# Kernel optimization log

Hardware: AMD Instinct MI355X
Metric: run time of the kernel (lower is better)

Reference implementation:

```python
import jax, jax.numpy as jnp
import numpy as np

N = 50000   # nodes
E = 800000  # edges
D = 256     # input feature dim
H = 128     # hidden size
OUT = 40    # output classes


def setup_inputs() -> dict:
    key = jax.random.key(0)
    ks = jax.random.split(key, 10)
    s = 0.05
    return {
        "x": jax.random.normal(ks[0], (N, D), jnp.float32),
        "edge_index": jax.random.randint(ks[1], (2, E), 0, N, dtype=jnp.int64),
        "W0": jax.random.normal(ks[2], (D, H), jnp.float32) * s,
        "b0": jnp.zeros((H,), jnp.float32),
        "W1": jax.random.normal(ks[3], (H, H), jnp.float32) * s,
        "b1": jnp.zeros((H,), jnp.float32),
        "W2": jax.random.normal(ks[4], (H, H), jnp.float32) * s,
        "b2": jnp.zeros((H,), jnp.float32),
        "Wout": jax.random.normal(ks[5], (H * 3, OUT), jnp.float32) * s,
        "bout": jnp.zeros((OUT,), jnp.float32),
    }


def _gcn_norm(edge_index, n):
    # PyG gcn_norm: add self-loops, symmetric D^-1/2 (A+I) D^-1/2 weights
    row, col = edge_index[0], edge_index[1]
    loop = jnp.arange(n, dtype=edge_index.dtype)
    row = jnp.concatenate([row, loop])
    col = jnp.concatenate([col, loop])
    deg = jax.ops.segment_sum(jnp.ones_like(col, jnp.float32), col, num_segments=n)
    dinv = jnp.where(deg > 0, jax.lax.rsqrt(jnp.maximum(deg, 1.0)), 0.0)
    norm = dinv[row] * dinv[col]  # [E+N]
    return row, col, norm


def _gcn_conv(x, W, b, row, col, norm, n):
    h = x @ W                                   # dense transform first (PyG order)
    msg = h[row] * norm[:, None]                # gather source feats, scale
    out = jax.ops.segment_sum(msg, col, num_segments=n)  # scatter-aggregate
    return out + b


def reference(x, edge_index, W0, b0, W1, b1, W2, b2, Wout, bout):
    n = x.shape[0]
    row, col, norm = _gcn_norm(edge_index, n)
    x1 = jax.nn.relu(_gcn_conv(x, W0, b0, row, col, norm, n))
    x2 = jax.nn.relu(_gcn_conv(x1, W1, b1, row, col, norm, n))
    x3 = jax.nn.relu(_gcn_conv(x2, W2, b2, row, col, norm, n))
    xs = jnp.concatenate([x1, x2, x3], axis=-1)  # JumpingKnowledge 'cat'
    return xs @ Wout + bout
```

## Files before the change

### kernel.cpp

```cpp
#include <hip/hip_runtime.h>

#define HID 128
#define NOUT 40
#define SCAN_B 256
#define NWIN 8

typedef __attribute__((ext_vector_type(8))) short bf16x8;
typedef __attribute__((ext_vector_type(4))) float f32x4;

__device__ inline float bf2f(unsigned int u) {
    unsigned int t = u << 16;
    float f;
    __builtin_memcpy(&f, &t, 4);
    return f;
}
__device__ inline unsigned short f2bf(float f) {
    unsigned int x;
    __builtin_memcpy(&x, &f, 4);
    unsigned int r = (x + 0x7fffu + ((x >> 16) & 1u)) >> 16;
    return (unsigned short)r;
}
__device__ inline bf16x8 pack_bf8(float4 u, float4 v) {
    bf16x8 r;
    r[0] = (short)f2bf(u.x); r[1] = (short)f2bf(u.y);
    r[2] = (short)f2bf(u.z); r[3] = (short)f2bf(u.w);
    r[4] = (short)f2bf(v.x); r[5] = (short)f2bf(v.y);
    r[6] = (short)f2bf(v.z); r[7] = (short)f2bf(v.w);
    return r;
}

__global__ void detect_fmt_kernel(const unsigned int* __restrict__ e, int* __restrict__ flag) {
    int t = threadIdx.x;
    unsigned int v = e[2 * t + 1];
    unsigned long long ball = __ballot(v == 0u);
    if (t == 0) *flag = (ball == ~0ull) ? 1 : 0;
}

__global__ void degree_kernel(const void* __restrict__ eix, const int* __restrict__ flag,
                              int* __restrict__ deg, int E) {
    int i = blockIdx.x * blockDim.x + threadIdx.x;
    if (i >= E) return;
    int f = *flag;
    int c = f ? (int)(((const long long*)eix)[(size_t)E + i]) : ((const int*)eix)[(size_t)E + i];
    atomicAdd(&deg[c], 1);
}

__global__ void scan1_kernel(const int* __restrict__ deg, int* __restrict__ offs,
                             int* __restrict__ bsum, float* __restrict__ dinv, int N) {
    __shared__ int s[SCAN_B];
    int i = blockIdx.x * SCAN_B + threadIdx.x;
    int v = (i < N) ? deg[i] : 0;
    if (i < N) dinv[i] = rsqrtf((float)v + 1.0f);
    s[threadIdx.x] = v;
    __syncthreads();
    for (int d = 1; d < SCAN_B; d <<= 1) {
        int t = (threadIdx.x >= d) ? s[threadIdx.x - d] : 0;
        __syncthreads();
        s[threadIdx.x] += t;
        __syncthreads();
    }
    if (i < N) offs[i] = s[threadIdx.x] - v;
    if (threadIdx.x == SCAN_B - 1) bsum[blockIdx.x] = s[SCAN_B - 1];
}

__global__ void scan2_kernel(int* __restrict__ bsum, int nb) {
    __shared__ int s[SCAN_B];
    int v = (threadIdx.x < nb) ? bsum[threadIdx.x] : 0;
    s[threadIdx.x] = v;
    __syncthreads();
    for (int d = 1; d < SCAN_B; d <<= 1) {
        int t = (threadIdx.x >= d) ? s[threadIdx.x - d] : 0;
        __syncthreads();
        s[threadIdx.x] += t;
        __syncthreads();
    }
    if (threadIdx.x < nb) bsum[threadIdx.x] = s[threadIdx.x] - v;
}

__global__ void scan3_kernel(int* __restrict__ offs, const int* __restrict__ bsum,
                             int* __restrict__ cursor, int N, int E) {
    int i = blockIdx.x * SCAN_B + threadIdx.x;
    if (i < N) {
        int v = offs[i] + bsum[blockIdx.x];
        offs[i] = v;
        cursor[i] = v;
    }
    if (blockIdx.x == 0 && threadIdx.x == 0) offs[N] = E;
}

__global__ __launch_bounds__(256) void fill_csr_kernel(
    const void* __restrict__ eix, const int* __restrict__ flag,
    const float* __restrict__ dinv, int* __restrict__ cursor,
    int2* __restrict__ pkd, int E, int N) {
    const int wn = blockIdx.x & (NWIN - 1);
    const int slice = blockIdx.x >> 3;
    const int nslice = gridDim.x >> 3;
    const int wsz = (N + NWIN - 1) / NWIN;
    const int lo = wn * wsz, hi = lo + wsz;
    const int f = *flag;
    const int stride = nslice * 256;
    for (int i = slice * 256 + threadIdx.x; i < E; i += stride) {
        int r, c;
        if (f) {
            r = (int)(((const long long*)eix)[i]);
            c = (int)(((const long long*)eix)[(size_t)E + i]);
        } else {
            r = ((const int*)eix)[i];
            c = ((const int*)eix)[(size_t)E + i];
        }
        if (c >= lo && c < hi) {
            int p = atomicAdd(&cursor[c], 1);
            int2 rec;
            rec.x = r;
            rec.y = __float_as_int(dinv[r] * dinv[c]);
            pkd[p] = rec;
        }
    }
}

__global__ void wt_all_kernel(const float* __restrict__ W0, const float* __restrict__ W1,
                              const float* __restrict__ W2, const float* __restrict__ Wo,
                              unsigned short* __restrict__ W0t, unsigned short* __restrict__ W1t,
                              unsigned short* __restrict__ W2t, unsigned short* __restrict__ Wot) {
    int idx = blockIdx.x * blockDim.x + threadIdx.x;
    const int s0 = 128 * 256, s1 = 128 * 128, s2 = 128 * 128, s3 = 48 * 384;
    if (idx < s0) {
        int n = idx >> 8, k = idx & 255;
        W0t[idx] = f2bf(W0[(size_t)k * 128 + n]);
    } else if ((idx -= s0) < s1) {
        int n = idx >> 7, k = idx & 127;
        W1t[idx] = f2bf(W1[(size_t)k * 128 + n]);
    } else if ((idx -= s1) < s2) {
        int n = idx >> 7, k = idx & 127;
        W2t[idx] = f2bf(W2[(size_t)k * 128 + n]);
    } else if ((idx -= s2) < s3) {
        int n = idx / 384, k = idx - n * 384;
        Wot[idx] = (n < NOUT) ? f2bf(Wo[(size_t)k * NOUT + n]) : (unsigned short)0;
    }
}

template <bool AF32>
__global__ __launch_bounds__(256) void gemm_mfma_kernel(
    const void* __restrict__ Ap, const unsigned short* __restrict__ Wt,
    unsigned short* __restrict__ H, int M, int K) {
    const int tid = threadIdx.x;
    const int lane = tid & 63;
    const int w = tid >> 6;
    const int lr = lane & 15;
    const int ko = lane >> 4;
    const int bm = blockIdx.x * 64;

    f32x4 acc[8];
#pragma unroll
    for (int j = 0; j < 8; ++j) acc[j] = (f32x4){0.f, 0.f, 0.f, 0.f};

    int R = bm + w * 16 + lr;
    if (R >= M) R = M - 1;
    const size_t aoff = (size_t)R * K + ko * 8;
    size_t boff[8];
#pragma unroll
    for (int ni = 0; ni < 8; ++ni) boff[ni] = (size_t)(ni * 16 + lr) * K + ko * 8;

#pragma unroll 4
    for (int k0 = 0; k0 < K; k0 += 32) {
        bf16x8 a, b[8];
        if constexpr (AF32) {
            const float* p = (const float*)Ap + aoff + k0;
            float4 u = *(const float4*)p;
            float4 v = *(const float4*)(p + 4);
            a = pack_bf8(u, v);
        } else {
            a = *(const bf16x8*)((const unsigned short*)Ap + aoff + k0);
        }
#pragma unroll
        for (int ni = 0; ni < 8; ++ni) b[ni] = *(const bf16x8*)(Wt + boff[ni] + k0);
#pragma unroll
        for (int ni = 0; ni < 8; ++ni)
            acc[ni] = __builtin_amdgcn_mfma_f32_16x16x32_bf16(a, b[ni], acc[ni], 0, 0, 0);
    }

    const int Rb = bm + w * 16 + ko * 4;
#pragma unroll
    for (int r = 0; r < 4; ++r) {
        int Ro = Rb + r;
        if (Ro < M) {
#pragma unroll
            for (int ni = 0; ni < 8; ++ni) {
                int C = ni * 16 + lr;
                H[(size_t)Ro * HID + C] = f2bf(acc[ni][r]);
            }
        }
    }
}

__global__ __launch_bounds__(256) void agg_csr_kernel(
    const unsigned int* __restrict__ h32, const int* __restrict__ offs,
    const int2* __restrict__ pkd, const float* __restrict__ dinv,
    const float* __restrict__ bias, unsigned int* __restrict__ xo, int N) {
    const int lane = threadIdx.x & 63;
    const int n = (blockIdx.x * blockDim.x + threadIdx.x) >> 6;
    if (n >= N) return;
    const float d = dinv[n];
    unsigned int sv = h32[(size_t)n * 64 + lane];
    float ax = bf2f(sv & 0xffff) * (d * d) + bias[2 * lane + 0];
    float ay = bf2f(sv >> 16) * (d * d) + bias[2 * lane + 1];
    int e = offs[n];
    const int e1 = offs[n + 1];

    for (; e + 16 <= e1; e += 16) {
        int2 pk[16];
        unsigned int v[16];
#pragma unroll
        for (int j = 0; j < 16; ++j) pk[j] = pkd[e + j];
#pragma unroll
        for (int j = 0; j < 16; ++j) v[j] = h32[(size_t)pk[j].x * 64 + lane];
#pragma unroll
        for (int j = 0; j < 16; ++j) {
            float wv = __int_as_float(pk[j].y);
            ax += bf2f(v[j] & 0xffff) * wv;
            ay += bf2f(v[j] >> 16) * wv;
        }
    }
    for (; e + 4 <= e1; e += 4) {
        int2 pk[4];
        unsigned int v[4];
#pragma unroll
        for (int j = 0; j < 4; ++j) pk[j] = pkd[e + j];
#pragma unroll
        for (int j = 0; j < 4; ++j) v[j] = h32[(size_t)pk[j].x * 64 + lane];
#pragma unroll
        for (int j = 0; j < 4; ++j) {
            float wv = __int_as_float(pk[j].y);
            ax += bf2f(v[j] & 0xffff) * wv;
            ay += bf2f(v[j] >> 16) * wv;
        }
    }
    for (; e < e1; ++e) {
        int2 pk = pkd[e];
        unsigned int v = h32[(size_t)pk.x * 64 + lane];
        float wv = __int_as_float(pk.y);
        ax += bf2f(v & 0xffff) * wv;
        ay += bf2f(v >> 16) * wv;
    }
    ax = fmaxf(ax, 0.f);
    ay = fmaxf(ay, 0.f);
    xo[(size_t)n * 64 + lane] = (unsigned int)f2bf(ax) | ((unsigned int)f2bf(ay) << 16);
}

__global__ __launch_bounds__(256) void head_mfma_kernel(
    const unsigned short* __restrict__ x1, const unsigned short* __restrict__ x2,
    const unsigned short* __restrict__ x3, const unsigned short* __restrict__ Wt,
    const float* __restrict__ bout, float* __restrict__ out, int M) {
    const int tid = threadIdx.x;
    const int lane = tid & 63;
    const int w = tid >> 6;
    const int lr = lane & 15;
    const int ko = lane >> 4;
    const int bm = blockIdx.x * 64;
    int R = bm + w * 16 + lr;
    if (R >= M) R = M - 1;
    const unsigned short* xs[3] = {x1, x2, x3};

    f32x4 acc[3];
#pragma unroll
    for (int i = 0; i < 3; ++i) acc[i] = (f32x4){0.f, 0.f, 0.f, 0.f};

#pragma unroll
    for (int s = 0; s < 3; ++s) {
        const unsigned short* xp = xs[s] + (size_t)R * HID + ko * 8;
#pragma unroll
        for (int c = 0; c < 4; ++c) {
            bf16x8 a = *(const bf16x8*)(xp + c * 32);
#pragma unroll
            for (int ni = 0; ni < 3; ++ni) {
                bf16x8 b = *(const bf16x8*)(Wt + (size_t)(ni * 16 + lr) * 384 + s * 128 + c * 32 + ko * 8);
                acc[ni] = __builtin_amdgcn_mfma_f32_16x16x32_bf16(a, b, acc[ni], 0, 0, 0);
            }
        }
    }

    int Rb = bm + w * 16 + ko * 4;
#pragma unroll
    for (int r = 0; r < 4; ++r) {
        int Ro = Rb + r;
        if (Ro < M) {
#pragma unroll
            for (int ni = 0; ni < 3; ++ni) {
                int C = ni * 16 + lr;
                if (C < NOUT) out[(size_t)Ro * NOUT + C] = acc[ni][r] + bout[C];
            }
        }
    }
}

static inline size_t align_up(size_t x, size_t a) { return (x + a - 1) / a * a; }

extern "C" void kernel_launch(void* const* d_in, const int* in_sizes, int n_in,
                              void* d_out, int out_size, void* d_ws, size_t ws_size,
                              hipStream_t stream) {
    const float* x    = (const float*)d_in[0];
    const void*  eix  = d_in[1];
    const float* W0   = (const float*)d_in[2];
    const float* b0   = (const float*)d_in[3];
    const float* W1   = (const float*)d_in[4];
    const float* b1   = (const float*)d_in[5];
    const float* W2   = (const float*)d_in[6];
    const float* b2   = (const float*)d_in[7];
    const float* Wout = (const float*)d_in[8];
    const float* bout = (const float*)d_in[9];
    float* out = (float*)d_out;

    const int D = 256;
    const int N = in_sizes[0] / D;
    const int E = in_sizes[1] / 2;

    char* w = (char*)d_ws;
    size_t off = 0;
    int* deg = (int*)(w + off);             off = align_up(off + (size_t)N * 4, 256);
    float* dinv = (float*)(w + off);        off = align_up(off + (size_t)N * 4, 256);
    int* offs = (int*)(w + off);            off = align_up(off + (size_t)(N + 1) * 4, 256);
    int* cursor = (int*)(w + off);          off = align_up(off + (size_t)N * 4, 256);
    int* bsum = (int*)(w + off);            off = align_up(off + 1024 * 4, 256);
    int* flag = (int*)(w + off);            off = align_up(off + 16, 256);
    int2* pkd = (int2*)(w + off);           off = align_up(off + (size_t)E * 8, 256);
    unsigned short* h   = (unsigned short*)(w + off); off = align_up(off + (size_t)N * HID * 2, 256);
    unsigned short* x1b = (unsigned short*)(w + off); off = align_up(off + (size_t)N * HID * 2, 256);
    unsigned short* x2b = (unsigned short*)(w + off); off = align_up(off + (size_t)N * HID * 2, 256);
    unsigned short* x3b = (unsigned short*)(w + off); off = align_up(off + (size_t)N * HID * 2, 256);
    unsigned short* W0t = (unsigned short*)(w + off); off = align_up(off + (size_t)HID * 256 * 2, 256);
    unsigned short* W1t = (unsigned short*)(w + off); off = align_up(off + (size_t)HID * HID * 2, 256);
    unsigned short* W2t = (unsigned short*)(w + off); off = align_up(off + (size_t)HID * HID * 2, 256);
    unsigned short* Wot = (unsigned short*)(w + off); off = align_up(off + (size_t)48 * 384 * 2, 256);
    (void)ws_size;

    detect_fmt_kernel<<<1, 64, 0, stream>>>((const unsigned int*)eix, flag);
    hipMemsetAsync(deg, 0, (size_t)N * 4, stream);
    degree_kernel<<<(E + 255) / 256, 256, 0, stream>>>(eix, flag, deg, E);

    const int nb = (N + SCAN_B - 1) / SCAN_B;
    scan1_kernel<<<nb, SCAN_B, 0, stream>>>(deg, offs, bsum, dinv, N);
    scan2_kernel<<<1, SCAN_B, 0, stream>>>(bsum, nb);
    scan3_kernel<<<nb, SCAN_B, 0, stream>>>(offs, bsum, cursor, N, E);
    fill_csr_kernel<<<NWIN * 256, 256, 0, stream>>>(eix, flag, dinv, cursor, pkd, E, N);

    const int wtTot = 128 * 256 + 128 * 128 + 128 * 128 + 48 * 384;
    wt_all_kernel<<<(wtTot + 255) / 256, 256, 0, stream>>>(W0, W1, W2, Wout, W0t, W1t, W2t, Wot);

    const int gGemm = (N + 63) / 64;
    const int gAgg = (N * 64 + 255) / 256;

    gemm_mfma_kernel<true><<<gGemm, 256, 0, stream>>>(x, W0t, h, N, 256);
    agg_csr_kernel<<<gAgg, 256, 0, stream>>>((const unsigned int*)h, offs, pkd, dinv, b0, (unsigned int*)x1b, N);
    gemm_mfma_kernel<false><<<gGemm, 256, 0, stream>>>(x1b, W1t, h, N, HID);
    agg_csr_kernel<<<gAgg, 256, 0, stream>>>((const unsigned int*)h, offs, pkd, dinv, b1, (unsigned int*)x2b, N);
    gemm_mfma_kernel<false><<<gGemm, 256, 0, stream>>>(x2b, W2t, h, N, HID);
    agg_csr_kernel<<<gAgg, 256, 0, stream>>>((const unsigned int*)h, offs, pkd, dinv, b2, (unsigned int*)x3b, N);
    head_mfma_kernel<<<gGemm, 256, 0, stream>>>(x1b, x2b, x3b, Wot, bout, out, N);
}
```

Measured before the change: 404.2 us.

## Stage GEMM weights in swizzled LDS, double M-tile, coalesce output via LDS

```diff
diff --git a/kernel.cpp b/kernel.cpp
--- a/kernel.cpp
+++ b/kernel.cpp
@@ -139,55 +139,86 @@
     }
 }
 
-template <bool AF32>
+template <bool AF32, int K>
 __global__ __launch_bounds__(256) void gemm_mfma_kernel(
     const void* __restrict__ Ap, const unsigned short* __restrict__ Wt,
-    unsigned short* __restrict__ H, int M, int K) {
+    unsigned short* __restrict__ H, int M) {
+    constexpr int NCH = K / 8;
+    __shared__ unsigned short Bs[128 * K];
     const int tid = threadIdx.x;
     const int lane = tid & 63;
     const int w = tid >> 6;
     const int lr = lane & 15;
     const int ko = lane >> 4;
-    const int bm = blockIdx.x * 64;
-
-    f32x4 acc[8];
-#pragma unroll
-    for (int j = 0; j < 8; ++j) acc[j] = (f32x4){0.f, 0.f, 0.f, 0.f};
-
-    int R = bm + w * 16 + lr;
-    if (R >= M) R = M - 1;
-    const size_t aoff = (size_t)R * K + ko * 8;
-    size_t boff[8];
-#pragma unroll
-    for (int ni = 0; ni < 8; ++ni) boff[ni] = (size_t)(ni * 16 + lr) * K + ko * 8;
+    const int bm = blockIdx.x * 128;
+
+    for (int c = tid; c < 128 * NCH; c += 256) {
+        int row = c / NCH;
+        int ch = c - row * NCH;
+        int sch = ch ^ (row & 7);
+        *(bf16x8*)(Bs + row * K + sch * 8) = *(const bf16x8*)(Wt + (size_t)row * K + ch * 8);
+    }
+    __syncthreads();
+
+    f32x4 acc[2][8];
+#pragma unroll
+    for (int i = 0; i < 2; ++i)
+#pragma unroll
+        for (int j = 0; j < 8; ++j) acc[i][j] = (f32x4){0.f, 0.f, 0.f, 0.f};
+
+    size_t aoff[2];
+#pragma unroll
+    for (int mi = 0; mi < 2; ++mi) {
+        int R = bm + w * 32 + mi * 16 + lr;
+        if (R >= M) R = M - 1;
+        aoff[mi] = (size_t)R * K + ko * 8;
+    }
 
 #pragma unroll 4
     for (int k0 = 0; k0 < K; k0 += 32) {
-        bf16x8 a, b[8];
-        if constexpr (AF32) {
-            const float* p = (const float*)Ap + aoff + k0;
-            float4 u = *(const float4*)p;
-            float4 v = *(const float4*)(p + 4);
-            a = pack_bf8(u, v);
-        } else {
-            a = *(const bf16x8*)((const unsigned short*)Ap + aoff + k0);
-        }
-#pragma unroll
-        for (int ni = 0; ni < 8; ++ni) b[ni] = *(const bf16x8*)(Wt + boff[ni] + k0);
+        bf16x8 a[2], b[8];
+#pragma unroll
+        for (int mi = 0; mi < 2; ++mi) {
+            if constexpr (AF32) {
+                const float* p = (const float*)Ap + aoff[mi] + k0;
+                float4 u = *(const float4*)p;
+                float4 v = *(const float4*)(p + 4);
+                a[mi] = pack_bf8(u, v);
+            } else {
+                a[mi] = *(const bf16x8*)((const unsigned short*)Ap + aoff[mi] + k0);
+            }
+        }
+        const int chb = (k0 >> 3) + ko;
+#pragma unroll
+        for (int ni = 0; ni < 8; ++ni) {
+            int row = ni * 16 + lr;
+            b[ni] = *(const bf16x8*)(Bs + row * K + ((chb ^ (row & 7)) * 8));
+        }
+#pragma unroll
+        for (int mi = 0; mi < 2; ++mi)
+#pragma unroll
+            for (int ni = 0; ni < 8; ++ni)
+                acc[mi][ni] = __builtin_amdgcn_mfma_f32_16x16x32_bf16(a[mi], b[ni], acc[mi][ni], 0, 0, 0);
+    }
+
+    __syncthreads();
+    unsigned short* Cw = Bs + w * (16 * 136);
+#pragma unroll
+    for (int mi = 0; mi < 2; ++mi) {
 #pragma unroll
         for (int ni = 0; ni < 8; ++ni)
-            acc[ni] = __builtin_amdgcn_mfma_f32_16x16x32_bf16(a, b[ni], acc[ni], 0, 0, 0);
-    }
-
-    const int Rb = bm + w * 16 + ko * 4;
-#pragma unroll
-    for (int r = 0; r < 4; ++r) {
-        int Ro = Rb + r;
-        if (Ro < M) {
-#pragma unroll
-            for (int ni = 0; ni < 8; ++ni) {
-                int C = ni * 16 + lr;
-                H[(size_t)Ro * HID + C] = f2bf(acc[ni][r]);
+#pragma unroll
+            for (int r = 0; r < 4; ++r)
+                Cw[(ko * 4 + r) * 136 + ni * 16 + lr] = f2bf(acc[mi][ni][r]);
+        const int R0 = bm + w * 32 + mi * 16;
+#pragma unroll
+        for (int p = 0; p < 4; ++p) {
+            int row = p * 4 + (lane >> 4);
+            int col = (lane & 15) * 8;
+            int Ro = R0 + row;
+            if (Ro < M) {
+                uint4 v = *(const uint4*)(Cw + row * 136 + col);
+                *(uint4*)(H + (size_t)Ro * HID + col) = v;
             }
         }
     }
@@ -346,14 +377,14 @@
     const int wtTot = 128 * 256 + 128 * 128 + 128 * 128 + 48 * 384;
     wt_all_kernel<<<(wtTot + 255) / 256, 256, 0, stream>>>(W0, W1, W2, Wout, W0t, W1t, W2t, Wot);
 
-    const int gGemm = (N + 63) / 64;
+    const int gGemm = (N + 127) / 128;
     const int gAgg = (N * 64 + 255) / 256;
 
-    gemm_mfma_kernel<true><<<gGemm, 256, 0, stream>>>(x, W0t, h, N, 256);
+    gemm_mfma_kernel<true, 256><<<gGemm, 256, 0, stream>>>(x, W0t, h, N);
     agg_csr_kernel<<<gAgg, 256, 0, stream>>>((const unsigned int*)h, offs, pkd, dinv, b0, (unsigned int*)x1b, N);
-    gemm_mfma_kernel<false><<<gGemm, 256, 0, stream>>>(x1b, W1t, h, N, HID);
+    gemm_mfma_kernel<false, 128><<<gGemm, 256, 0, stream>>>(x1b, W1t, h, N);
     agg_csr_kernel<<<gAgg, 256, 0, stream>>>((const unsigned int*)h, offs, pkd, dinv, b1, (unsigned int*)x2b, N);
-    gemm_mfma_kernel<false><<<gGemm, 256, 0, stream>>>(x2b, W2t, h, N, HID);
+    gemm_mfma_kernel<false, 128><<<gGemm, 256, 0, stream>>>(x2b, W2t, h, N);
     agg_csr_kernel<<<gAgg, 256, 0, stream>>>((const unsigned int*)h, offs, pkd, dinv, b2, (unsigned int*)x3b, N);
-    head_mfma_kernel<<<gGemm, 256, 0, stream>>>(x1b, x2b, x3b, Wot, bout, out, N);
-}
+    head_mfma_kernel<<<(N + 63) / 64, 256, 0, stream>>>(x1b, x2b, x3b, Wot, bout, out, N);
+}
```

Measured after the change: 361.3 us. 1.12x faster.
